# Optimization experiments

Measured on AMD Instinct MI355X. Metric: run time of the kernel, lower is better.

Reference implementation:

```python
import jax, jax.numpy as jnp
import numpy as np

B, T, H = 4, 512, 768
N, S = 256, 16
NER_DIM = 32
D = H + NER_DIM  # node_in_dim = 800
L, R = 2, 15
NE, MM = 64, 8
P = 1024
E = 4096
OUT = 97
NER_NUM = 7


def setup_inputs() -> dict:
    key = jax.random.key(0)
    ks = jax.random.split(key, 20)
    f = jax.random.normal
    inp = {}
    inp['token_feature'] = f(ks[0], (B, T, H), jnp.float32)
    inp['doc_cls_feature'] = f(ks[1], (B, H), jnp.float32)
    inp['node_span_pos'] = jax.random.randint(ks[2], (B, N, S), 0, T)
    inp['node_span_mask'] = jnp.ones((B, N, S), jnp.float32)
    inp['node_ner'] = jax.random.randint(ks[3], (B, N), 0, NER_NUM + 1)
    inp['node_mask'] = jnp.ones((B, N), jnp.float32)
    inp['ent2MentionId'] = jax.random.randint(ks[4], (B, NE, MM), 0, N + 1)
    inp['ent2MentionId_mask'] = jnp.ones((B, NE, MM), jnp.float32)
    inp['ent_pair'] = jax.random.randint(ks[5], (B, P, 2), 0, NE)
    inp['edge_src'] = jax.random.randint(ks[6], (B, E), 0, N)
    inp['edge_dst'] = jax.random.randint(ks[7], (B, E), 0, N)
    inp['edge_rel'] = jax.random.randint(ks[8], (B, E), 0, R)
    inp['ment_num'] = jax.random.randint(ks[9], (B,), 0, N)
    s = lambda k, sh: f(k, sh, jnp.float32) * 0.02
    inp['nerEmb'] = s(ks[10], (NER_NUM + 1, NER_DIM))
    inp['doc_W'] = s(ks[11], (H, D))
    inp['doc_b'] = jnp.zeros((D,), jnp.float32)
    inp['W_rel'] = s(ks[12], (L, R, D, D))
    inp['W_self'] = s(ks[13], (L, D, D))
    inp['gnn_b'] = jnp.zeros((L, D), jnp.float32)
    EE = 2 * D  # entity_embed_dim = 1600
    inp['W1'] = s(ks[14], (4 * EE, 2 * EE))
    inp['b1'] = jnp.zeros((2 * EE,), jnp.float32)
    inp['W2'] = s(ks[15], (2 * EE, OUT))
    inp['b2'] = jnp.zeros((OUT,), jnp.float32)
    return inp


def reference(token_feature, doc_cls_feature, node_span_pos, node_span_mask, node_ner,
              node_mask, ent2MentionId, ent2MentionId_mask, ent_pair, edge_src,
              edge_dst, edge_rel, ment_num, nerEmb, doc_W, doc_b, W_rel, W_self,
              gnn_b, W1, b1, W2, b2):
    # span pooling: gather span tokens, masked mean (avg pool with +0.1 denom as in source)
    span_tok = jax.vmap(lambda tf, p: tf[p])(token_feature, node_span_pos)  # [B,N,S,H]
    span = (span_tok * node_span_mask[..., None]).sum(2)
    span = span / (node_span_mask.sum(2, keepdims=True) + 0.1)
    node = span + doc_cls_feature[:, None, :]  # use_doc_feature add
    doc_proj = jax.nn.relu(doc_cls_feature @ doc_W + doc_b)  # doc_feature_fc
    node = jnp.concatenate([node, nerEmb[node_ner]], -1) * node_mask[..., None]  # [B,N,D]

    def per_sample(x, docp, m, src, dst, rel, e2m, e2m_mask, pairs):
        # node_in_feature[ment_num] = doc_cls_feature
        x = x.at[m].set(docp)
        outs = []
        h = x
        for l in range(L):
            # relational graph conv: per-relation transform then gather-scatter over edges
            Hr = jnp.einsum('nd,rde->rne', h, W_rel[l])  # [R,N,D]
            msg = Hr[rel, src]                            # [E,D]
            agg = jax.ops.segment_sum(msg, dst, num_segments=N)
            h = jax.nn.relu(agg + h @ W_self[l] + gnn_b[l])
            outs.append(h)
        on = jnp.concatenate([outs[0], outs[-1]], -1)     # [N,2D]
        on = jnp.concatenate([jnp.zeros((1, on.shape[-1]), on.dtype), on], 0)  # pad row 0
        ent = (on[e2m] * e2m_mask[..., None]).sum(1) / (e2m_mask.sum(1, keepdims=True) + 1e-7)
        hf = ent[pairs[:, 0]]
        tf_ = ent[pairs[:, 1]]
        feat = jnp.concatenate([hf, tf_, jnp.abs(hf - tf_), hf * tf_], -1)  # [P,4*EE]
        return jax.nn.relu(feat @ W1 + b1) @ W2 + b2       # [P,OUT]

    return jax.vmap(per_sample)(node, doc_proj, ment_num, edge_src, edge_dst,
                                edge_rel, ent2MentionId, ent2MentionId_mask, ent_pair)
```

## Files before the change

kernel.cpp:

```cpp
#include <hip/hip_runtime.h>
#include <hip/hip_bf16.h>

#define B_    4
#define T_    512
#define H_    768
#define N_    256
#define S_    16
#define NERD  32
#define D_    800
#define L_    2
#define R_    15
#define NE_   64
#define MM_   8
#define P_    1024
#define E_    4096
#define OUT_  97
#define NW    12800
#define EE2   1600
#define KF    (4 * EE2)
#define NH    (2 * EE2)
#define KS    800
#define NZ    4

typedef unsigned short u16;
typedef unsigned int   u32;
typedef __attribute__((ext_vector_type(8))) short  short8;
typedef __attribute__((ext_vector_type(4))) float  f32x4;

#define AS1 __attribute__((address_space(1)))
#define AS3 __attribute__((address_space(3)))

static __device__ __forceinline__ u16 f2bf(float f) {
  union { float f; u32 u; } v; v.f = f;
  u32 u = v.u;
  u32 r = (u + 0x7FFFu + ((u >> 16) & 1u)) >> 16;
  return (u16)r;
}
static __device__ __forceinline__ float bf2f(u16 h) {
  union { u32 u; float f; } v; v.u = ((u32)h) << 16;
  return v.f;
}

__global__ __launch_bounds__(256) void k_doc_proj(
    const float* __restrict__ doc_cls, const float* __restrict__ doc_W,
    const float* __restrict__ doc_b, float* __restrict__ doc_proj) {
  int i = blockIdx.x * 256 + threadIdx.x;
  if (i >= B_ * D_) return;
  int b = i / D_, d = i % D_;
  float acc = doc_b[d];
  const float* dc = doc_cls + b * H_;
#pragma unroll 4
  for (int k = 0; k < H_; k++) acc += dc[k] * doc_W[k * D_ + d];
  doc_proj[i] = fmaxf(acc, 0.f);
}

__global__ __launch_bounds__(256) void k_build_node(
    const float* __restrict__ tokf, const float* __restrict__ doc_cls,
    const int* __restrict__ span_pos, const float* __restrict__ span_mask,
    const int* __restrict__ node_ner, const float* __restrict__ node_mask,
    const int* __restrict__ ment_num, const float* __restrict__ nerEmb,
    const float* __restrict__ doc_proj, u16* __restrict__ xB) {
  int n = blockIdx.x, b = blockIdx.y;
  __shared__ int pos_s[S_];
  __shared__ float msk_s[S_];
  int tid = threadIdx.x;
  if (tid < S_) {
    pos_s[tid] = span_pos[((size_t)b * N_ + n) * S_ + tid];
    msk_s[tid] = span_mask[((size_t)b * N_ + n) * S_ + tid];
  }
  __syncthreads();
  float msum = 0.f;
#pragma unroll
  for (int s = 0; s < S_; s++) msum += msk_s[s];
  float rinv = 1.f / (msum + 0.1f);
  int m = ment_num[b];
  float nm = node_mask[b * N_ + n];
  int ner = node_ner[b * N_ + n];
  for (int d = tid; d < D_; d += 256) {
    float v;
    if (d < H_) {
      float ssum = 0.f;
#pragma unroll
      for (int s = 0; s < S_; s++)
        ssum += tokf[((size_t)b * T_ + pos_s[s]) * H_ + d] * msk_s[s];
      v = ssum * rinv + doc_cls[b * H_ + d];
    } else {
      v = nerEmb[ner * NERD + (d - H_)];
    }
    v *= nm;
    if (n == m) v = doc_proj[b * D_ + d];
    xB[((size_t)b * N_ + n) * D_ + d] = f2bf(v);
  }
}

__global__ __launch_bounds__(256) void k_wt(const float* __restrict__ W_rel,
                                            const float* __restrict__ W_self,
                                            u16* __restrict__ WT) {
  __shared__ float tile[32][33];
  int l = blockIdx.z >> 4, i = blockIdx.z & 15;
  const float* src = (i < 15) ? (W_rel + ((size_t)l * R_ + i) * D_ * D_)
                              : (W_self + (size_t)l * D_ * D_);
  u16* dst = WT + (size_t)l * NW * D_ + (size_t)i * D_ * D_;
  int d0 = blockIdx.x * 32, e0 = blockIdx.y * 32;
  int tx = threadIdx.x & 31, ty = threadIdx.x >> 5;
  for (int j = ty; j < 32; j += 8)
    tile[j][tx] = src[(size_t)(d0 + j) * D_ + e0 + tx];
  __syncthreads();
  for (int j = ty; j < 32; j += 8)
    dst[(size_t)(e0 + j) * D_ + d0 + tx] = f2bf(tile[tx][j]);
}

__global__ __launch_bounds__(256) void k_w1t(const float* __restrict__ W1,
                                             u16* __restrict__ W1abT,
                                             u16* __restrict__ W1cdT) {
  __shared__ float tile[32][33];
  int k0 = blockIdx.x * 32, n0 = blockIdx.y * 32;
  int tx = threadIdx.x & 31, ty = threadIdx.x >> 5;
  for (int i = ty; i < 32; i += 8)
    tile[i][tx] = W1[(size_t)(k0 + i) * NH + n0 + tx];
  __syncthreads();
  for (int i = ty; i < 32; i += 8) {
    int kk = k0 + tx, n = n0 + i;
    u16 v = f2bf(tile[tx][i]);
    if (kk < EE2)            W1abT[(size_t)n * EE2 + kk] = v;
    else if (kk < 2 * EE2)   W1abT[(size_t)(NH + n) * EE2 + (kk - EE2)] = v;
    else                     W1cdT[(size_t)n * NH + (kk - 2 * EE2)] = v;
  }
}

__global__ __launch_bounds__(256) void k_w2t(const float* __restrict__ W2,
                                             u16* __restrict__ W2T) {
  __shared__ float tile[32][33];
  int k0 = blockIdx.x * 32, n0 = blockIdx.y * 32;
  int tx = threadIdx.x & 31, ty = threadIdx.x >> 5;
  for (int i = ty; i < 32; i += 8)
    tile[i][tx] = (n0 + tx < OUT_) ? W2[(size_t)(k0 + i) * OUT_ + n0 + tx] : 0.f;
  __syncthreads();
  for (int i = ty; i < 32; i += 8)
    W2T[(size_t)(n0 + i) * NH + k0 + tx] = f2bf(tile[tx][i]);
}

__global__ __launch_bounds__(256) void k_csr_zero(int* __restrict__ cnt) {
  cnt[blockIdx.x * 256 + threadIdx.x] = 0;
}
__global__ __launch_bounds__(256) void k_csr_count(const int* __restrict__ edst,
                                                   int* __restrict__ cnt) {
  int e = blockIdx.x * 256 + threadIdx.x, b = blockIdx.y;
  atomicAdd(&cnt[b * N_ + edst[(size_t)b * E_ + e]], 1);
}
__global__ __launch_bounds__(256) void k_csr_scan(const int* __restrict__ cnt,
                                                  int* __restrict__ rowptr,
                                                  int* __restrict__ cursor) {
  int b = blockIdx.x, t = threadIdx.x;
  __shared__ int s[N_];
  int own = cnt[b * N_ + t];
  s[t] = own;
  __syncthreads();
  for (int off = 1; off < N_; off <<= 1) {
    int v = (t >= off) ? s[t - off] : 0;
    __syncthreads();
    s[t] += v;
    __syncthreads();
  }
  int excl = s[t] - own;
  rowptr[b * (N_ + 1) + t] = excl;
  cursor[b * N_ + t] = excl;
  if (t == 0) rowptr[b * (N_ + 1) + N_] = E_;
}
__global__ __launch_bounds__(256) void k_csr_fill(
    const int* __restrict__ esrc, const int* __restrict__ edst,
    const int* __restrict__ erel, int* __restrict__ cursor,
    int* __restrict__ elist) {
  int e = blockIdx.x * 256 + threadIdx.x, b = blockIdx.y;
  size_t ei = (size_t)b * E_ + e;
  int pos = atomicAdd(&cursor[b * N_ + edst[ei]], 1);
  elist[b * E_ + pos] = esrc[ei] | (erel[ei] << 9);
}

template <int KD, int EPI>
__global__ __launch_bounds__(256) void k_gemm_bt(
    const u16* __restrict__ A, int lda, const u16* __restrict__ Bm, int ldb,
    const float* __restrict__ bias, const float* __restrict__ preA,
    const float* __restrict__ preB, const int* __restrict__ pairs,
    void* __restrict__ Cv, int ldc, int ldpre, long long zA, long long zC) {
  __shared__ u16 As[128 * 32];
  __shared__ u16 Bs[128 * 32];
  int tid = threadIdx.x;
  int w = tid >> 6, lane = tid & 63;
  int wr = w >> 1, wc = w & 1;
  int lane16 = lane & 15, quad = lane >> 4;

  int nbn = gridDim.x, nbm = gridDim.y;
  int pid = blockIdx.y * nbn + blockIdx.x;
  const int GROUP = 8;
  int npg = GROUP * nbn;
  int gidg = pid / npg;
  int first = gidg * GROUP;
  int szm = min(nbm - first, GROUP);
  int pid_m = first + (pid % npg) % szm;
  int pid_n = (pid % npg) / szm;
  int n0 = pid_n * 128;
  int m0 = pid_m * 128;

  int lrow = lane >> 2;
  int lcol = (lane & 3) * 8;

  f32x4 acc[4][4] = {};

  const u16* gA = A + (size_t)blockIdx.z * zA + (size_t)m0 * lda;
  const u16* gB = Bm + (size_t)blockIdx.z * zA + (size_t)n0 * ldb;

  for (int kt = 0; kt < KD; kt += 32) {
    __syncthreads();
#pragma unroll
    for (int j = 0; j < 2; j++) {
      int chunk = j * 4 + w;
      int row = chunk * 16 + lrow;
      __builtin_amdgcn_global_load_lds(
          (const AS1 void*)(gA + (size_t)row * lda + kt + lcol),
          (AS3 void*)(As + chunk * 512 + lane * 8), 16, 0, 0);
      __builtin_amdgcn_global_load_lds(
          (const AS1 void*)(gB + (size_t)row * ldb + kt + lcol),
          (AS3 void*)(Bs + chunk * 512 + lane * 8), 16, 0, 0);
    }
    __syncthreads();

    short8 af[4], bf[4];
#pragma unroll
    for (int mi = 0; mi < 4; mi++) {
      int ml = wr * 64 + mi * 16 + lane16;
      af[mi] = *(const short8*)(As + ml * 32 + quad * 8);
    }
#pragma unroll
    for (int ni = 0; ni < 4; ni++) {
      int nl = wc * 64 + ni * 16 + lane16;
      bf[ni] = *(const short8*)(Bs + nl * 32 + quad * 8);
    }
#pragma unroll
    for (int mi = 0; mi < 4; mi++)
#pragma unroll
      for (int ni = 0; ni < 4; ni++)
        acc[mi][ni] = __builtin_amdgcn_mfma_f32_16x16x32_bf16(
            af[mi], bf[ni], acc[mi][ni], 0, 0, 0);
  }

  int cols[4];
  float bv[4];
#pragma unroll
  for (int ni = 0; ni < 4; ni++) {
    cols[ni] = n0 + wc * 64 + ni * 16 + lane16;
    if (EPI == 4) bv[ni] = (cols[ni] < NH) ? bias[cols[ni]] : 0.f;
  }
  float* Cf = (float*)Cv + (size_t)blockIdx.z * zC;
#pragma unroll
  for (int mi = 0; mi < 4; mi++) {
#pragma unroll
    for (int r = 0; r < 4; r++) {
      int row = m0 + wr * 64 + mi * 16 + quad * 4 + r;
      const float* pAr = nullptr;
      const float* pBr = nullptr;
      if (EPI == 2) {
        int hp = pairs[2 * row], tp = pairs[2 * row + 1];
        int pb = (row >> 10) * NE_;
        pAr = preA + (size_t)(pb + hp) * ldpre;
        pBr = preB + (size_t)(pb + tp) * ldpre;
      }
#pragma unroll
      for (int ni = 0; ni < 4; ni++) {
        float v = acc[mi][ni][r];
        int col = cols[ni];
        if (EPI == 0) {
          ((u16*)Cv)[(size_t)row * ldc + col] = f2bf(v);
        } else if (EPI == 1) {
          Cf[(size_t)row * ldc + col] = v;
        } else if (EPI == 2) {
          v += pAr[col] + pBr[col];
          ((u16*)Cv)[(size_t)row * ldc + col] = f2bf(fmaxf(v, 0.f));
        } else if (EPI == 4) {
          Cf[(size_t)row * ldc + col] = v + bv[ni];
        }
      }
    }
  }
}

__global__ __launch_bounds__(128) void k_out_reduce(
    const float* __restrict__ part, const float* __restrict__ b2,
    float* __restrict__ out) {
  int row = blockIdx.x, c = threadIdx.x;
  if (c >= OUT_) return;
  float s = b2[c];
#pragma unroll
  for (int z = 0; z < NZ; z++)
    s += part[(size_t)z * (B_ * P_ * 128) + (size_t)row * 128 + c];
  out[(size_t)row * OUT_ + c] = s;
}

__global__ __launch_bounds__(256) void k_agg(
    const u16* __restrict__ Hr, const int* __restrict__ rowptr,
    const int* __restrict__ elist, const float* __restrict__ gnn_b, int layer,
    float* __restrict__ hout, u16* __restrict__ houtB) {
  int n = blockIdx.x, b = blockIdx.y;
  int beg = rowptr[b * (N_ + 1) + n], end = rowptr[b * (N_ + 1) + n + 1];
  const int* el = elist + (size_t)b * E_;
  const u16* HrB = Hr + (size_t)b * N_ * NW;
  int tid = threadIdx.x;
  for (int c = tid; c < D_; c += 256) {
    float acc = bf2f(HrB[(size_t)n * NW + R_ * D_ + c]) + gnn_b[layer * D_ + c];
    for (int i = beg; i < end; i++) {
      int pk = el[i];
      acc += bf2f(HrB[(size_t)(pk & 511) * NW + (pk >> 9) * D_ + c]);
    }
    float r = fmaxf(acc, 0.f);
    hout[((size_t)b * N_ + n) * D_ + c] = r;
    houtB[((size_t)b * N_ + n) * D_ + c] = f2bf(r);
  }
}

__global__ __launch_bounds__(256) void k_ent(
    const float* __restrict__ h0, const float* __restrict__ h1,
    const int* __restrict__ e2m, const float* __restrict__ e2m_mask,
    float* __restrict__ ent, u16* __restrict__ entB) {
  int e = blockIdx.x, b = blockIdx.y;
  __shared__ int idx_s[MM_];
  __shared__ float msk_s[MM_];
  int tid = threadIdx.x;
  if (tid < MM_) {
    idx_s[tid] = e2m[((size_t)b * NE_ + e) * MM_ + tid];
    msk_s[tid] = e2m_mask[((size_t)b * NE_ + e) * MM_ + tid];
  }
  __syncthreads();
  float msum = 0.f;
#pragma unroll
  for (int m = 0; m < MM_; m++) msum += msk_s[m];
  float inv = 1.f / (msum + 1e-7f);
  for (int c = tid; c < EE2; c += 256) {
    const float* base = (c < D_) ? h0 : h1;
    int cc = (c < D_) ? c : c - D_;
    float s = 0.f;
#pragma unroll
    for (int m = 0; m < MM_; m++) {
      int j = idx_s[m];
      if (j > 0) s += base[((size_t)b * N_ + (j - 1)) * D_ + cc] * msk_s[m];
    }
    float v = s * inv;
    ent[((size_t)b * NE_ + e) * EE2 + c] = v;
    entB[((size_t)b * NE_ + e) * EE2 + c] = f2bf(v);
  }
}

__global__ __launch_bounds__(256) void k_featC(
    const float* __restrict__ ent, const int* __restrict__ ent_pair,
    u16* __restrict__ featC) {
  int row = blockIdx.x;
  int b = row >> 10, g = row & 1023;
  int hp = ent_pair[(((size_t)b << 10) + g) * 2 + 0];
  int tp = ent_pair[(((size_t)b << 10) + g) * 2 + 1];
  const float* eh = ent + ((size_t)b * NE_ + hp) * EE2;
  const float* et = ent + ((size_t)b * NE_ + tp) * EE2;
  u16* orow = featC + (size_t)row * NH;
  for (int c = threadIdx.x; c < 800; c += 256) {
    int seg = c / 400, kk = (c - seg * 400) * 4;
    float4 hf = *(const float4*)(eh + kk);
    float4 tf = *(const float4*)(et + kk);
    float4 v;
    if (seg == 0) {
      v.x = fabsf(hf.x - tf.x); v.y = fabsf(hf.y - tf.y);
      v.z = fabsf(hf.z - tf.z); v.w = fabsf(hf.w - tf.w);
    } else {
      v.x = hf.x * tf.x; v.y = hf.y * tf.y;
      v.z = hf.z * tf.z; v.w = hf.w * tf.w;
    }
    ushort4 o;
    o.x = f2bf(v.x); o.y = f2bf(v.y); o.z = f2bf(v.z); o.w = f2bf(v.w);
    *(ushort4*)(orow + seg * EE2 + kk) = o;
  }
}

extern "C" void kernel_launch(void* const* d_in, const int* in_sizes, int n_in,
                              void* d_out, int out_size, void* d_ws, size_t ws_size,
                              hipStream_t stream) {
  const float* token_feature = (const float*)d_in[0];
  const float* doc_cls       = (const float*)d_in[1];
  const int*   span_pos      = (const int*)d_in[2];
  const float* span_mask     = (const float*)d_in[3];
  const int*   node_ner      = (const int*)d_in[4];
  const float* node_mask     = (const float*)d_in[5];
  const int*   e2m           = (const int*)d_in[6];
  const float* e2m_mask      = (const float*)d_in[7];
  const int*   ent_pair      = (const int*)d_in[8];
  const int*   edge_src      = (const int*)d_in[9];
  const int*   edge_dst      = (const int*)d_in[10];
  const int*   edge_rel      = (const int*)d_in[11];
  const int*   ment_num      = (const int*)d_in[12];
  const float* nerEmb        = (const float*)d_in[13];
  const float* doc_W         = (const float*)d_in[14];
  const float* doc_b         = (const float*)d_in[15];
  const float* W_rel         = (const float*)d_in[16];
  const float* W_self        = (const float*)d_in[17];
  const float* gnn_b         = (const float*)d_in[18];
  const float* W1            = (const float*)d_in[19];
  const float* b1            = (const float*)d_in[20];
  const float* W2            = (const float*)d_in[21];
  const float* b2            = (const float*)d_in[22];
  float* out = (float*)d_out;

  float* ws = (float*)d_ws;
  size_t off = 0;
  auto alloc = [&](size_t n) {
    float* p = ws + off;
    off += (n + 63) & ~size_t(63);
    return p;
  };
  float* doc_proj = alloc(B_ * D_);
  u16*   xB  = (u16*)alloc((size_t)B_ * N_ * D_ / 2);
  float* h0  = alloc((size_t)B_ * N_ * D_);
  float* h1  = alloc((size_t)B_ * N_ * D_);
  u16*   hB  = (u16*)alloc((size_t)B_ * N_ * D_ / 2);
  float* ent = alloc((size_t)B_ * NE_ * EE2);
  u16*   entB = (u16*)alloc((size_t)B_ * NE_ * EE2 / 2);
  u16*   WT    = (u16*)alloc((size_t)L_ * NW * D_ / 2);
  u16*   W1abT = (u16*)alloc((size_t)KF * EE2 / 2);
  u16*   W1cdT = (u16*)alloc((size_t)NH * NH / 2);
  u16*   W2T   = (u16*)alloc((size_t)128 * NH / 2);
  float* preAB = alloc((size_t)B_ * NE_ * KF);
  u16*   Hr    = (u16*)alloc((size_t)B_ * N_ * NW / 2);
  u16*   featC = Hr;
  u16*   hiddenB = (u16*)alloc((size_t)B_ * P_ * NH / 2);
  float* part    = alloc((size_t)NZ * B_ * P_ * 128);
  int*   csr_cnt    = (int*)alloc(B_ * N_ / 1 * sizeof(int) / 4);
  int*   csr_rowptr = (int*)alloc(B_ * (N_ + 1));
  int*   csr_cursor = (int*)alloc(B_ * N_);
  int*   csr_elist  = (int*)alloc(B_ * E_);
  (void)ws_size;

  k_csr_zero<<<dim3(B_), 256, 0, stream>>>(csr_cnt);
  k_csr_count<<<dim3(E_ / 256, B_), 256, 0, stream>>>(edge_dst, csr_cnt);
  k_csr_scan<<<dim3(B_), 256, 0, stream>>>(csr_cnt, csr_rowptr, csr_cursor);
  k_csr_fill<<<dim3(E_ / 256, B_), 256, 0, stream>>>(edge_src, edge_dst, edge_rel,
                                                     csr_cursor, csr_elist);

  k_wt<<<dim3(D_ / 32, D_ / 32, L_ * 16), 256, 0, stream>>>(W_rel, W_self, WT);
  k_w1t<<<dim3(KF / 32, NH / 32), 256, 0, stream>>>(W1, W1abT, W1cdT);
  k_w2t<<<dim3(NH / 32, 4), 256, 0, stream>>>(W2, W2T);

  k_doc_proj<<<dim3((B_ * D_ + 255) / 256), 256, 0, stream>>>(doc_cls, doc_W, doc_b, doc_proj);
  k_build_node<<<dim3(N_, B_), 256, 0, stream>>>(token_feature, doc_cls, span_pos, span_mask,
                                                 node_ner, node_mask, ment_num, nerEmb,
                                                 doc_proj, xB);
  const u16* hin = xB;
  float* houts[2] = {h0, h1};
  for (int l = 0; l < L_; l++) {
    k_gemm_bt<D_, 0><<<dim3(NW / 128, (B_ * N_) / 128), 256, 0, stream>>>(
        hin, D_, WT + (size_t)l * NW * D_, D_, nullptr, nullptr, nullptr, nullptr,
        Hr, NW, 0, 0, 0);
    k_agg<<<dim3(N_, B_), 256, 0, stream>>>(Hr, csr_rowptr, csr_elist,
                                            gnn_b, l, houts[l], hB);
    hin = hB;
  }
  k_ent<<<dim3(NE_, B_), 256, 0, stream>>>(h0, h1, e2m, e2m_mask, ent, entB);

  k_gemm_bt<EE2, 4><<<dim3(KF / 128, (B_ * NE_) / 128), 256, 0, stream>>>(
      entB, EE2, W1abT, EE2, b1, nullptr, nullptr, nullptr, preAB, KF, 0, 0, 0);

  k_featC<<<dim3(B_ * P_), 256, 0, stream>>>(ent, ent_pair, featC);

  k_gemm_bt<NH, 2><<<dim3(NH / 128, (B_ * P_) / 128), 256, 0, stream>>>(
      featC, NH, W1cdT, NH, nullptr, preAB, preAB + NH, ent_pair, hiddenB, NH,
      KF, 0, 0);

  k_gemm_bt<KS, 1><<<dim3(1, (B_ * P_) / 128, NZ), 256, 0, stream>>>(
      hiddenB, NH, W2T, NH, nullptr, nullptr, nullptr, nullptr, part, 128,
      0, KS, (long long)B_ * P_ * 128);
  k_out_reduce<<<dim3(B_ * P_), 128, 0, stream>>>(part, b2, out);
}
```

Baseline: 786.9 us.

## Replace pair-feature GEMM with 256x256 pipelined direct-to-LDS MFMA kernel

The large featC x W1cd GEMM with its fused pre-activation add and ReLU epilogue now runs in a dedicated 512-thread kernel. It uses 256x256 output tiles, double-buffered global_load_lds staging into XOR-swizzled LDS, interleaved barriers with setprio around the MFMA groups, and a grouped block-index remap for L2 reuse. W1cdT is padded to 3328 rows and a new kernel zero-fills the extra rows so the N dimension divides by 256. The intent is more data reuse per tile and better overlap of loads with MFMA than the generic 128x128 kernel. The cost is higher register and LDS pressure, and the padded columns add wasted compute.

```diff
diff --git a/kernel.cpp b/kernel.cpp
--- a/kernel.cpp
+++ b/kernel.cpp
@@ -19,6 +19,7 @@
 #define EE2   1600
 #define KF    (4 * EE2)
 #define NH    (2 * EE2)
+#define NPAD  3328
 #define KS    800
 #define NZ    4
 
@@ -128,6 +129,11 @@
   }
 }
 
+__global__ __launch_bounds__(256) void k_w1cd_pad(u16* __restrict__ W1cdT) {
+  size_t i = (size_t)blockIdx.x * 256 + threadIdx.x;
+  ((u32*)(W1cdT + (size_t)NH * NH))[i] = 0u;
+}
+
 __global__ __launch_bounds__(256) void k_w2t(const float* __restrict__ W2,
                                              u16* __restrict__ W2T) {
   __shared__ float tile[32][33];
@@ -257,14 +263,6 @@
 #pragma unroll
     for (int r = 0; r < 4; r++) {
       int row = m0 + wr * 64 + mi * 16 + quad * 4 + r;
-      const float* pAr = nullptr;
-      const float* pBr = nullptr;
-      if (EPI == 2) {
-        int hp = pairs[2 * row], tp = pairs[2 * row + 1];
-        int pb = (row >> 10) * NE_;
-        pAr = preA + (size_t)(pb + hp) * ldpre;
-        pBr = preB + (size_t)(pb + tp) * ldpre;
-      }
 #pragma unroll
       for (int ni = 0; ni < 4; ni++) {
         float v = acc[mi][ni][r];
@@ -273,11 +271,163 @@
           ((u16*)Cv)[(size_t)row * ldc + col] = f2bf(v);
         } else if (EPI == 1) {
           Cf[(size_t)row * ldc + col] = v;
-        } else if (EPI == 2) {
-          v += pAr[col] + pBr[col];
-          ((u16*)Cv)[(size_t)row * ldc + col] = f2bf(fmaxf(v, 0.f));
         } else if (EPI == 4) {
           Cf[(size_t)row * ldc + col] = v + bv[ni];
+        }
+      }
+    }
+  }
+}
+
+__global__ __launch_bounds__(512, 2) void k_gemm8p(
+    const u16* __restrict__ A, const u16* __restrict__ Bm,
+    const float* __restrict__ preAB_, const int* __restrict__ pairs,
+    u16* __restrict__ C) {
+  __shared__ u16 lds[2][2][2][128 * 64];
+
+  int tid = threadIdx.x;
+  int w = tid >> 6, lane = tid & 63;
+  int wr = w >> 2, wc = w & 3;
+  int lane16 = lane & 15, quad = lane >> 4;
+
+  int pid = blockIdx.y * 13 + blockIdx.x;
+  pid = (pid & 7) * 26 + (pid >> 3);
+  int pid_m = pid / 13, pid_n = pid % 13;
+  int m0 = pid_m * 256, n0 = pid_n * 256;
+
+  int srow = (w << 3) + (lane >> 3);
+  int g8 = ((lane & 7) ^ (lane >> 3)) << 3;
+  const u16* gAt = A + (size_t)(m0 + srow) * NH + g8;
+  const u16* gBt = Bm + (size_t)(n0 + srow) * NH + g8;
+  int ldsSlot = ((w << 6) + lane) << 3;
+
+#define STAGE(buf, ab, h, kt)                                                  \
+  do {                                                                         \
+    const u16* gsrc_ = (ab) ? gBt : gAt;                                       \
+    __builtin_amdgcn_global_load_lds(                                          \
+        (const AS1 void*)(gsrc_ + (size_t)((h)*128) * NH + (kt)),              \
+        (AS3 void*)(&lds[buf][ab][h][0] + ldsSlot), 16, 0, 0);                 \
+    __builtin_amdgcn_global_load_lds(                                          \
+        (const AS1 void*)(gsrc_ + (size_t)((h)*128 + 64) * NH + (kt)),         \
+        (AS3 void*)(&lds[buf][ab][h][0] + 4096 + ldsSlot), 16, 0, 0);          \
+  } while (0)
+
+  auto rdA = [&](int buf, int mi, int ks) {
+    int rh = mi * 16 + lane16;
+    int p = ((ks << 2) + quad) ^ (lane16 & 7);
+    return *(const short8*)(&lds[buf][0][wr][(rh << 6) + (p << 3)]);
+  };
+  auto rdB = [&](int buf, int ni, int ks) {
+    int rh = (wc & 1) * 64 + ni * 16 + lane16;
+    int p = ((ks << 2) + quad) ^ (lane16 & 7);
+    return *(const short8*)(&lds[buf][1][wc >> 1][(rh << 6) + (p << 3)]);
+  };
+
+  f32x4 acc[8][4] = {};
+  short8 a_[8][2];
+  short8 b0_[4];
+  short8 b1_[4];
+
+  STAGE(0, 0, 0, 0); STAGE(0, 0, 1, 0); STAGE(0, 1, 0, 0); STAGE(0, 1, 1, 0);
+  STAGE(1, 0, 0, 64); STAGE(1, 0, 1, 64); STAGE(1, 1, 0, 64);
+  asm volatile("s_waitcnt vmcnt(6)" ::: "memory");
+  __builtin_amdgcn_s_barrier();
+
+  const int NIT = NH / 128;
+  for (int it = 0; it < NIT; ++it) {
+    const int kbase = it * 128;
+    const int kB1 = kbase + 64;
+    const int kp2 = (it < NIT - 1) ? kbase + 128 : 0;
+    const int kp3 = (it < NIT - 1) ? kbase + 192 : 0;
+#pragma unroll
+    for (int hv = 0; hv < 2; ++hv) {
+#pragma unroll
+      for (int mi = 0; mi < 8; ++mi) {
+        a_[mi][0] = rdA(hv, mi, 0);
+        a_[mi][1] = rdA(hv, mi, 1);
+      }
+#pragma unroll
+      for (int ni = 0; ni < 4; ++ni) b0_[ni] = rdB(hv, ni, 0);
+      if (hv == 0) { STAGE(1, 1, 1, kB1); } else { STAGE(0, 1, 1, kp2); }
+      asm volatile("" ::: "memory");
+      __builtin_amdgcn_s_barrier();
+      asm volatile("s_waitcnt lgkmcnt(0)" ::: "memory");
+      __builtin_amdgcn_sched_barrier(0);
+      __builtin_amdgcn_s_setprio(1);
+#pragma unroll
+      for (int mi = 0; mi < 8; ++mi) {
+        acc[mi][0] = __builtin_amdgcn_mfma_f32_16x16x32_bf16(a_[mi][0], b0_[0], acc[mi][0], 0, 0, 0);
+        acc[mi][1] = __builtin_amdgcn_mfma_f32_16x16x32_bf16(a_[mi][0], b0_[1], acc[mi][1], 0, 0, 0);
+      }
+      __builtin_amdgcn_s_setprio(0);
+      asm volatile("" ::: "memory");
+      __builtin_amdgcn_s_barrier();
+
+#pragma unroll
+      for (int ni = 0; ni < 4; ++ni) b1_[ni] = rdB(hv, ni, 1);
+      if (hv == 0) { STAGE(0, 0, 0, kp2); } else { STAGE(1, 0, 0, kp3); }
+      asm volatile("" ::: "memory");
+      __builtin_amdgcn_s_barrier();
+      asm volatile("s_waitcnt lgkmcnt(0)" ::: "memory");
+      __builtin_amdgcn_sched_barrier(0);
+      __builtin_amdgcn_s_setprio(1);
+#pragma unroll
+      for (int mi = 0; mi < 8; ++mi) {
+        acc[mi][2] = __builtin_amdgcn_mfma_f32_16x16x32_bf16(a_[mi][0], b0_[2], acc[mi][2], 0, 0, 0);
+        acc[mi][3] = __builtin_amdgcn_mfma_f32_16x16x32_bf16(a_[mi][0], b0_[3], acc[mi][3], 0, 0, 0);
+      }
+      __builtin_amdgcn_s_setprio(0);
+      asm volatile("" ::: "memory");
+      __builtin_amdgcn_s_barrier();
+
+      if (hv == 0) { STAGE(0, 0, 1, kp2); } else { STAGE(1, 0, 1, kp3); }
+      asm volatile("" ::: "memory");
+      __builtin_amdgcn_s_barrier();
+      asm volatile("s_waitcnt lgkmcnt(0)" ::: "memory");
+      __builtin_amdgcn_sched_barrier(0);
+      __builtin_amdgcn_s_setprio(1);
+#pragma unroll
+      for (int mi = 0; mi < 8; ++mi) {
+        acc[mi][0] = __builtin_amdgcn_mfma_f32_16x16x32_bf16(a_[mi][1], b1_[0], acc[mi][0], 0, 0, 0);
+        acc[mi][1] = __builtin_amdgcn_mfma_f32_16x16x32_bf16(a_[mi][1], b1_[1], acc[mi][1], 0, 0, 0);
+      }
+      __builtin_amdgcn_s_setprio(0);
+      asm volatile("" ::: "memory");
+      __builtin_amdgcn_s_barrier();
+
+      if (hv == 0) { STAGE(0, 1, 0, kp2); } else { STAGE(1, 1, 0, kp3); }
+      asm volatile("" ::: "memory");
+      __builtin_amdgcn_s_barrier();
+      asm volatile("s_waitcnt lgkmcnt(0)" ::: "memory");
+      __builtin_amdgcn_sched_barrier(0);
+      __builtin_amdgcn_s_setprio(1);
+#pragma unroll
+      for (int mi = 0; mi < 8; ++mi) {
+        acc[mi][2] = __builtin_amdgcn_mfma_f32_16x16x32_bf16(a_[mi][1], b1_[2], acc[mi][2], 0, 0, 0);
+        acc[mi][3] = __builtin_amdgcn_mfma_f32_16x16x32_bf16(a_[mi][1], b1_[3], acc[mi][3], 0, 0, 0);
+      }
+      __builtin_amdgcn_s_setprio(0);
+      asm volatile("s_waitcnt vmcnt(6)" ::: "memory");
+      __builtin_amdgcn_s_barrier();
+    }
+  }
+#undef STAGE
+
+#pragma unroll
+  for (int mi = 0; mi < 8; ++mi) {
+#pragma unroll
+    for (int r = 0; r < 4; ++r) {
+      int row = m0 + wr * 128 + mi * 16 + quad * 4 + r;
+      int hp = pairs[2 * row], tp = pairs[2 * row + 1];
+      int pb = (row >> 10) * NE_;
+      const float* pAr = preAB_ + (size_t)(pb + hp) * KF;
+      const float* pBr = preAB_ + NH + (size_t)(pb + tp) * KF;
+#pragma unroll
+      for (int ni = 0; ni < 4; ++ni) {
+        int col = n0 + wc * 64 + ni * 16 + lane16;
+        if (col < NH) {
+          float v = acc[mi][ni][r] + pAr[col] + pBr[col];
+          C[(size_t)row * NH + col] = f2bf(fmaxf(v, 0.f));
         }
       }
     }
@@ -421,7 +571,7 @@
   u16*   entB = (u16*)alloc((size_t)B_ * NE_ * EE2 / 2);
   u16*   WT    = (u16*)alloc((size_t)L_ * NW * D_ / 2);
   u16*   W1abT = (u16*)alloc((size_t)KF * EE2 / 2);
-  u16*   W1cdT = (u16*)alloc((size_t)NH * NH / 2);
+  u16*   W1cdT = (u16*)alloc((size_t)NPAD * NH / 2);
   u16*   W2T   = (u16*)alloc((size_t)128 * NH / 2);
   float* preAB = alloc((size_t)B_ * NE_ * KF);
   u16*   Hr    = (u16*)alloc((size_t)B_ * N_ * NW / 2);
@@ -442,6 +592,7 @@
 
   k_wt<<<dim3(D_ / 32, D_ / 32, L_ * 16), 256, 0, stream>>>(W_rel, W_self, WT);
   k_w1t<<<dim3(KF / 32, NH / 32), 256, 0, stream>>>(W1, W1abT, W1cdT);
+  k_w1cd_pad<<<dim3(800), 256, 0, stream>>>(W1cdT);
   k_w2t<<<dim3(NH / 32, 4), 256, 0, stream>>>(W2, W2T);
 
   k_doc_proj<<<dim3((B_ * D_ + 255) / 256), 256, 0, stream>>>(doc_cls, doc_W, doc_b, doc_proj);
@@ -465,9 +616,8 @@
 
   k_featC<<<dim3(B_ * P_), 256, 0, stream>>>(ent, ent_pair, featC);
 
-  k_gemm_bt<NH, 2><<<dim3(NH / 128, (B_ * P_) / 128), 256, 0, stream>>>(
-      featC, NH, W1cdT, NH, nullptr, preAB, preAB + NH, ent_pair, hiddenB, NH,
-      KF, 0, 0);
+  k_gemm8p<<<dim3(NPAD / 256, (B_ * P_) / 256), 512, 0, stream>>>(
+      featC, W1cdT, preAB, ent_pair, hiddenB);
 
   k_gemm_bt<KS, 1><<<dim3(1, (B_ * P_) / 128, NZ), 256, 0, stream>>>(
       hiddenB, NH, W2T, NH, nullptr, nullptr, nullptr, nullptr, part, 128,
```

Measured after the change: 784.3 us. No clear change (-0.3%).
